# Kernel tuning notes

Measured on AMD Instinct MI355X. Metric: run time of the kernel, lower is better.

## Reference

```python
import jax, jax.numpy as jnp
import numpy as np

B, N, Mdim, CS, INP, OUT = 256, 2048, 64, 512, 256, 256
ADDR_R = Mdim + 6          # k(M), beta(1), g(1), s(3), gamma(1)
ADDR_W = 3 * Mdim + 6      # + erase(M) + add(M)


def setup_inputs() -> dict:
    key = jax.random.key(0)
    ks = jax.random.split(key, 16)
    s = 0.05
    x = jax.random.normal(ks[0], (B, INP), dtype=jnp.float32)
    memory = jax.random.uniform(ks[1], (B, N, Mdim), dtype=jnp.float32) * 0.1 + 1e-6
    h = jax.random.normal(ks[2], (B, CS), dtype=jnp.float32) * 0.1
    c = jax.random.normal(ks[3], (B, CS), dtype=jnp.float32) * 0.1
    rw = jax.random.uniform(ks[4], (B, N), dtype=jnp.float32)
    read_w = rw / rw.sum(axis=1, keepdims=True)
    ww = jax.random.uniform(ks[5], (B, N), dtype=jnp.float32)
    write_w = ww / ww.sum(axis=1, keepdims=True)
    prev_read = jax.random.normal(ks[6], (B, Mdim), dtype=jnp.float32) * 0.1
    W_ih = jax.random.normal(ks[7], (4 * CS, INP + Mdim), dtype=jnp.float32) * s
    W_hh = jax.random.normal(ks[8], (4 * CS, CS), dtype=jnp.float32) * s
    b_ih = jnp.zeros((4 * CS,), jnp.float32)
    b_hh = jnp.zeros((4 * CS,), jnp.float32)
    W_r = jax.random.normal(ks[9], (ADDR_R, CS), dtype=jnp.float32) * s
    b_r = jnp.zeros((ADDR_R,), jnp.float32)
    W_w = jax.random.normal(ks[10], (ADDR_W, CS), dtype=jnp.float32) * s
    b_w = jnp.zeros((ADDR_W,), jnp.float32)
    W_o = jax.random.normal(ks[11], (OUT, CS + Mdim), dtype=jnp.float32) * s
    b_o = jnp.zeros((OUT,), jnp.float32)
    return dict(x=x, memory=memory, h=h, c=c, read_w=read_w, write_w=write_w,
                prev_read=prev_read, W_ih=W_ih, W_hh=W_hh, b_ih=b_ih, b_hh=b_hh,
                W_r=W_r, b_r=b_r, W_w=W_w, b_w=b_w, W_o=W_o, b_o=b_o)


def _addressing(out_vec, prev_w, memory, M):
    # Eq. 5-9: content softmax, interpolation, circular shift, sharpening.
    k = out_vec[:, :M]                                   # [B, M]
    beta = jax.nn.softplus(out_vec[:, M:M + 1])          # [B, 1]
    g = jax.nn.sigmoid(out_vec[:, M + 1:M + 2])          # [B, 1]
    s = jax.nn.softmax(out_vec[:, M + 2:M + 5], axis=1)  # [B, 3]
    gamma = 1.0 + jax.nn.softplus(out_vec[:, M + 5:M + 6])
    norm_k = jnp.linalg.norm(k, axis=1, keepdims=True) + 1e-8        # [B, 1]
    norm_mem = jnp.linalg.norm(memory, axis=2) + 1e-8                # [B, N]
    sim = jnp.einsum('bnm,bm->bn', memory, k) / (norm_k * norm_mem)  # cosine
    w_c = jax.nn.softmax(beta * sim, axis=1)
    w_g = g * w_c + (1.0 - g) * prev_w
    # circular convolution with 3-tap shift kernel (replaces the roll loop)
    w_s = (s[:, 0:1] * jnp.roll(w_g, 1, axis=1)
           + s[:, 1:2] * w_g
           + s[:, 2:3] * jnp.roll(w_g, -1, axis=1))
    w_pow = w_s ** gamma
    return w_pow / (w_pow.sum(axis=1, keepdims=True) + 1e-8)


def reference(x, memory, h, c, read_w, write_w, prev_read,
              W_ih, W_hh, b_ih, b_hh, W_r, b_r, W_w, b_w, W_o, b_o):
    M = memory.shape[2]
    inp = jnp.concatenate([x, prev_read], axis=1)
    gates = inp @ W_ih.T + b_ih + h @ W_hh.T + b_hh
    i_g, f_g, g_g, o_g = jnp.split(gates, 4, axis=1)  # torch LSTMCell gate order
    i_g = jax.nn.sigmoid(i_g); f_g = jax.nn.sigmoid(f_g)
    g_g = jnp.tanh(g_g); o_g = jax.nn.sigmoid(o_g)
    c_new = f_g * c + i_g * g_g
    h_new = o_g * jnp.tanh(c_new)
    # read head (uses pre-write memory)
    read_out = h_new @ W_r.T + b_r
    w_read = _addressing(read_out, read_w, memory, M)
    read_vec = jnp.einsum('bn,bnm->bm', w_read, memory)
    # write head: address, then erase/add outer-product update
    write_out = h_new @ W_w.T + b_w
    w_write = _addressing(write_out, write_w, memory, M)
    erase = jax.nn.sigmoid(write_out[:, M + 6:2 * M + 6])
    add = write_out[:, 2 * M + 6:3 * M + 6]
    memory_new = memory * (1.0 - w_write[:, :, None] * erase[:, None, :]) \
                 + w_write[:, :, None] * add[:, None, :]
    out = jnp.concatenate([h_new, read_vec], axis=1) @ W_o.T + b_o
    return (out, memory_new, h_new, c_new, w_read, w_write, read_vec)
```

## Files before the change

kernel.cpp:

```cpp
#include <hip/hip_runtime.h>
#include <math.h>

#define Bsz   256
#define Nn    2048
#define Md    64
#define CSd   512
#define INPd  256
#define OUTd  256
#define KTOT  832
#define PSTRIDE 272
#define GSZ   524288
#define ZSPL  4
#define KZ    208

__device__ __forceinline__ float sigmoidf_(float x){ return 1.f/(1.f+expf(-x)); }
__device__ __forceinline__ float softplusf_(float x){ return fmaxf(x,0.f) + log1pf(expf(-fabsf(x))); }

__device__ __forceinline__ float4 loadA4(const float* __restrict__ x, const float* __restrict__ pr,
                                         const float* __restrict__ h, int row, int k){
  if (k < INPd)            return *(const float4*)&x[row*INPd + k];
  else if (k < INPd+Md)    return *(const float4*)&pr[row*Md + (k-INPd)];
  else                     return *(const float4*)&h[row*CSd + (k-INPd-Md)];
}
__device__ __forceinline__ float4 loadW4(const float* __restrict__ Wih, const float* __restrict__ Whh,
                                         int j, int k){
  if (k < INPd+Md)         return *(const float4*)&Wih[j*(INPd+Md) + k];
  else                     return *(const float4*)&Whh[j*CSd + (k-INPd-Md)];
}

__global__ __launch_bounds__(256) void k_gates(
    const float* __restrict__ x, const float* __restrict__ prev_read, const float* __restrict__ h,
    const float* __restrict__ W_ih, const float* __restrict__ W_hh,
    float* __restrict__ partials)
{
  __shared__ __align__(16) float As[16][68];
  __shared__ __align__(16) float Bs[16][68];
  const int t = threadIdx.x;
  const int col0 = blockIdx.x * 64;
  const int row0 = blockIdx.y * 64;
  const int z    = blockIdx.z;
  const int lr = t >> 2;
  const int kq = (t & 3) * 4;
  const int tr = t >> 4, tc = t & 15;
  const int arow = row0 + lr;
  const int bcol = col0 + lr;

  float acc[4][4] = {};
  int kb = z * KZ;
  float4 a  = loadA4(x, prev_read, h, arow, kb + kq);
  float4 bq = loadW4(W_ih, W_hh, bcol, kb + kq);

  for (int kc = 0; kc < 13; ++kc) {
    As[kq+0][lr] = a.x;  As[kq+1][lr] = a.y;  As[kq+2][lr] = a.z;  As[kq+3][lr] = a.w;
    Bs[kq+0][lr] = bq.x; Bs[kq+1][lr] = bq.y; Bs[kq+2][lr] = bq.z; Bs[kq+3][lr] = bq.w;
    __syncthreads();
    if (kc < 12) {
      int kn = kb + (kc+1)*16 + kq;
      a  = loadA4(x, prev_read, h, arow, kn);
      bq = loadW4(W_ih, W_hh, bcol, kn);
    }
    #pragma unroll
    for (int kk = 0; kk < 16; ++kk) {
      float av[4], bv[4];
      *(float4*)&av[0] = *(const float4*)&As[kk][tr*4];
      *(float4*)&bv[0] = *(const float4*)&Bs[kk][tc*4];
      #pragma unroll
      for (int i=0;i<4;++i)
        #pragma unroll
        for (int q=0;q<4;++q)
          acc[i][q] += av[i]*bv[q];
    }
    __syncthreads();
  }
  float* part = partials + (size_t)z * GSZ;
  #pragma unroll
  for (int i=0;i<4;++i) {
    int r = row0 + tr*4 + i;
    float4 v0 = {acc[i][0],acc[i][1],acc[i][2],acc[i][3]};
    *(float4*)&part[r*2048 + col0 + tc*4] = v0;
  }
}

__global__ __launch_bounds__(512) void k_lstm_heads(
    const float* __restrict__ partials, const float* __restrict__ c,
    const float* __restrict__ b_ih, const float* __restrict__ b_hh,
    const float* __restrict__ W_r, const float* __restrict__ b_r,
    const float* __restrict__ W_w, const float* __restrict__ b_w,
    float* __restrict__ h_new, float* __restrict__ c_new, float* __restrict__ params)
{
  __shared__ float hs[CSd];
  __shared__ float ob[268];
  int b = blockIdx.x, t = threadIdx.x;
  float g[4];
  #pragma unroll
  for (int q = 0; q < 4; ++q) {
    int col = q*512 + t;
    float s = b_ih[col] + b_hh[col];
    #pragma unroll
    for (int sp = 0; sp < ZSPL; ++sp) s += partials[(size_t)sp*GSZ + b*2048 + col];
    g[q] = s;
  }
  float ig = sigmoidf_(g[0]);
  float fg = sigmoidf_(g[1]);
  float gg = tanhf(g[2]);
  float og = sigmoidf_(g[3]);
  float cn = fg * c[b*CSd + t] + ig * gg;
  float hn = og * tanhf(cn);
  c_new[b*CSd + t] = cn;
  h_new[b*CSd + t] = hn;
  hs[t] = hn;
  __syncthreads();
  int wave = t >> 6, lane = t & 63;
  for (int r = wave; r < 268; r += 8) {
    const float* wrow; float bias;
    if (r < 70) { wrow = W_r + r*CSd;      bias = b_r[r]; }
    else        { wrow = W_w + (r-70)*CSd; bias = b_w[r-70]; }
    float s = 0.f;
    #pragma unroll
    for (int i = 0; i < 8; ++i) s += wrow[i*64 + lane] * hs[i*64 + lane];
    #pragma unroll
    for (int off = 32; off; off >>= 1) s += __shfl_xor(s, off);
    if (lane == 0) ob[r] = s + bias;
  }
  __syncthreads();
  float* P = params + b*PSTRIDE;
  if (t < 256) {
    if (t < 64)       P[t] = ob[t];
    else if (t < 128) P[t] = ob[70 + (t-64)];
    else if (t < 192) P[t] = sigmoidf_(ob[140 + (t-128)]);
    else              P[t] = ob[204 + (t-192)];
  }
  float* S = P + 256;
  if (wave == 0) {
    float v = ob[lane]; float sq = v*v;
    #pragma unroll
    for (int off = 32; off; off >>= 1) sq += __shfl_xor(sq, off);
    if (lane == 0) S[6] = 1.f/(sqrtf(sq)+1e-8f);
  } else if (wave == 1) {
    float v = ob[70 + lane]; float sq = v*v;
    #pragma unroll
    for (int off = 32; off; off >>= 1) sq += __shfl_xor(sq, off);
    if (lane == 0) S[13] = 1.f/(sqrtf(sq)+1e-8f);
  }
  if (t == 128) {
    S[0] = softplusf_(ob[64]);
    S[1] = sigmoidf_(ob[65]);
    float m3 = fmaxf(ob[66], fmaxf(ob[67], ob[68]));
    float e0=expf(ob[66]-m3), e1=expf(ob[67]-m3), e2=expf(ob[68]-m3);
    float es = e0+e1+e2;
    S[2]=e0/es; S[3]=e1/es; S[4]=e2/es;
    S[5] = 1.f + softplusf_(ob[69]);
  }
  if (t == 129) {
    S[7] = softplusf_(ob[134]);
    S[8] = sigmoidf_(ob[135]);
    float m3 = fmaxf(ob[136], fmaxf(ob[137], ob[138]));
    float e0=expf(ob[136]-m3), e1=expf(ob[137]-m3), e2=expf(ob[138]-m3);
    float es = e0+e1+e2;
    S[9]=e0/es; S[10]=e1/es; S[11]=e2/es;
    S[12] = 1.f + softplusf_(ob[139]);
  }
}

__global__ __launch_bounds__(256) void k_sim(
    const float* __restrict__ mem, const float* __restrict__ params,
    float* __restrict__ a_r, float* __restrict__ a_w)
{
  int b = blockIdx.y;
  int n0 = blockIdx.x * 64;
  int rr = threadIdx.x >> 4;
  int chunk = threadIdx.x & 15;
  const float* P = params + b*PSTRIDE;
  float4 kr = ((const float4*)P)[chunk];
  float4 kw = ((const float4*)(P+64))[chunk];
  const float* S = P + 256;
  float cr = S[0] * S[6];
  float cw = S[7] * S[13];
  #pragma unroll
  for (int p = 0; p < 4; ++p) {
    int n = n0 + p*16 + rr;
    float4 v = ((const float4*)mem)[(b*Nn + n)*16 + chunk];
    float ss = v.x*v.x + v.y*v.y + v.z*v.z + v.w*v.w;
    float pr = v.x*kr.x + v.y*kr.y + v.z*kr.z + v.w*kr.w;
    float pw = v.x*kw.x + v.y*kw.y + v.z*kw.z + v.w*kw.w;
    #pragma unroll
    for (int off=8; off; off>>=1) {
      ss += __shfl_xor(ss, off);
      pr += __shfl_xor(pr, off);
      pw += __shfl_xor(pw, off);
    }
    if (chunk == 0) {
      float inv_nm = 1.f/(sqrtf(ss)+1e-8f);
      a_r[b*Nn+n] = cr * pr * inv_nm;
      a_w[b*Nn+n] = cw * pw * inv_nm;
    }
  }
}

__device__ __forceinline__ float block_reduce512(float val, float* red, int t, bool ismax){
  #pragma unroll
  for (int off=32; off; off>>=1)
    val = ismax ? fmaxf(val, __shfl_xor(val,off)) : val + __shfl_xor(val,off);
  __syncthreads();
  if ((t&63)==0) red[t>>6] = val;
  __syncthreads();
  float r = red[0];
  if (ismax) { for (int i=1;i<8;++i) r = fmaxf(r, red[i]); }
  else       { for (int i=1;i<8;++i) r += red[i]; }
  return r;
}

__global__ __launch_bounds__(512) void k_weights(
    const float* __restrict__ a_r, const float* __restrict__ a_w,
    const float* __restrict__ read_w, const float* __restrict__ write_w,
    const float* __restrict__ params,
    float* __restrict__ w_read, float* __restrict__ w_write)
{
  __shared__ float wg[Nn];
  __shared__ float red[8];
  int b = blockIdx.x;
  int which = blockIdx.y;
  const float* a    = which ? a_w     : a_r;
  const float* prev = which ? write_w : read_w;
  float* outw       = which ? w_write : w_read;
  const float* S = params + b*PSTRIDE + 256 + (which ? 7 : 0);
  float g = S[1], s0 = S[2], s1 = S[3], s2 = S[4], gamma = S[5];
  int t = threadIdx.x;
  float v[4];
  #pragma unroll
  for (int i=0;i<4;++i) v[i] = a[b*Nn + t*4+i];
  float lmax = fmaxf(fmaxf(v[0],v[1]), fmaxf(v[2],v[3]));
  float mx = block_reduce512(lmax, red, t, true);
  float e[4]; float ps = 0.f;
  #pragma unroll
  for (int i=0;i<4;++i){ e[i] = expf(v[i]-mx); ps += e[i]; }
  float denom = block_reduce512(ps, red, t, false);
  float inv = 1.f/denom;
  #pragma unroll
  for (int i=0;i<4;++i){
    float wc = e[i]*inv;
    wg[t*4+i] = g*wc + (1.f-g)*prev[b*Nn + t*4+i];
  }
  __syncthreads();
  float wp[4]; float psum = 0.f;
  #pragma unroll
  for (int i=0;i<4;++i){
    int n = t*4+i;
    float wsv = s0*wg[(n+Nn-1)&(Nn-1)] + s1*wg[n] + s2*wg[(n+1)&(Nn-1)];
    wp[i] = powf(wsv, gamma);
    psum += wp[i];
  }
  float tot = block_reduce512(psum, red, t, false);
  float invt = 1.f/(tot + 1e-8f);
  #pragma unroll
  for (int i=0;i<4;++i) outw[b*Nn + t*4+i] = wp[i]*invt;
}

__global__ __launch_bounds__(256) void k_memupd(
    const float* __restrict__ mem, const float* __restrict__ params,
    const float* __restrict__ w_read, const float* __restrict__ w_write,
    float* __restrict__ mem_new, float* __restrict__ prv)
{
  __shared__ __align__(16) float er[64];
  __shared__ __align__(16) float ad[64];
  __shared__ float4 part[64];
  int b = blockIdx.y;
  int n0 = blockIdx.x * 64;
  int t = threadIdx.x;
  const float* P = params + b*PSTRIDE;
  if (t < 64)       er[t]    = P[128+t];
  else if (t < 128) ad[t-64] = P[192+(t-64)];
  __syncthreads();
  int chunk = t & 15;
  int rr = t >> 4;
  float4 e4 = ((const float4*)er)[chunk];
  float4 a4 = ((const float4*)ad)[chunk];
  float4 acc = {0.f,0.f,0.f,0.f};
  #pragma unroll
  for (int p = 0; p < 4; ++p) {
    int n = n0 + p*16 + rr;
    float4 v = ((const float4*)mem)[(b*Nn+n)*16 + chunk];
    float ww = w_write[b*Nn+n];
    float wr = w_read[b*Nn+n];
    float4 o;
    o.x = v.x*(1.f-ww*e4.x) + ww*a4.x;
    o.y = v.y*(1.f-ww*e4.y) + ww*a4.y;
    o.z = v.z*(1.f-ww*e4.z) + ww*a4.z;
    o.w = v.w*(1.f-ww*e4.w) + ww*a4.w;
    ((float4*)mem_new)[(b*Nn+n)*16 + chunk] = o;
    acc.x += wr*v.x; acc.y += wr*v.y; acc.z += wr*v.z; acc.w += wr*v.w;
  }
  #pragma unroll
  for (int off = 16; off <= 32; off <<= 1) {
    acc.x += __shfl_xor(acc.x, off);
    acc.y += __shfl_xor(acc.y, off);
    acc.z += __shfl_xor(acc.z, off);
    acc.w += __shfl_xor(acc.w, off);
  }
  int wave = t >> 6;
  if ((t & 63) < 16) part[wave*16 + chunk] = acc;
  __syncthreads();
  if (t < 16) {
    float4 s = part[t];
    for (int w=1; w<4; ++w){ float4 q = part[w*16+t]; s.x+=q.x; s.y+=q.y; s.z+=q.z; s.w+=q.w; }
    *(float4*)&prv[(b*32 + blockIdx.x)*64 + t*4] = s;
  }
}

__global__ __launch_bounds__(256) void k_out(
    const float* __restrict__ h_new, const float* __restrict__ prv,
    const float* __restrict__ W_o, const float* __restrict__ b_o,
    float* __restrict__ out, float* __restrict__ read_vec)
{
  __shared__ float vbuf[576];
  int b = blockIdx.y, t = threadIdx.x;
  vbuf[t]     = h_new[b*CSd + t];
  vbuf[t+256] = h_new[b*CSd + t + 256];
  if (t < 64) {
    float s = 0.f;
    #pragma unroll 8
    for (int i = 0; i < 32; ++i) s += prv[(b*32 + i)*64 + t];
    vbuf[512+t] = s;
    if (blockIdx.x == 0) read_vec[b*64 + t] = s;
  }
  __syncthreads();
  int wave = t >> 6, lane = t & 63;
  float vb[9];
  #pragma unroll
  for (int i = 0; i < 9; ++i) vb[i] = vbuf[i*64 + lane];
  int cbase = blockIdx.x*64 + wave*16;
  for (int jj = 0; jj < 16; ++jj) {
    int cc = cbase + jj;
    const float* w = W_o + cc*576;
    float s = 0.f;
    #pragma unroll
    for (int i = 0; i < 9; ++i) s += w[i*64 + lane] * vb[i];
    #pragma unroll
    for (int off = 32; off; off >>= 1) s += __shfl_xor(s, off);
    if (lane == 0) out[b*OUTd + cc] = s + b_o[cc];
  }
}

extern "C" void kernel_launch(void* const* d_in, const int* in_sizes, int n_in,
                              void* d_out, int out_size, void* d_ws, size_t ws_size,
                              hipStream_t stream)
{
  const float* x         = (const float*)d_in[0];
  const float* memory    = (const float*)d_in[1];
  const float* h         = (const float*)d_in[2];
  const float* c         = (const float*)d_in[3];
  const float* read_w    = (const float*)d_in[4];
  const float* write_w   = (const float*)d_in[5];
  const float* prev_read = (const float*)d_in[6];
  const float* W_ih      = (const float*)d_in[7];
  const float* W_hh      = (const float*)d_in[8];
  const float* b_ih      = (const float*)d_in[9];
  const float* b_hh      = (const float*)d_in[10];
  const float* W_r       = (const float*)d_in[11];
  const float* b_r       = (const float*)d_in[12];
  const float* W_w       = (const float*)d_in[13];
  const float* b_w       = (const float*)d_in[14];
  const float* W_o       = (const float*)d_in[15];
  const float* b_o       = (const float*)d_in[16];

  float* out      = (float*)d_out;
  float* mem_new  = out + 256*256;
  float* h_new    = mem_new + (size_t)256*2048*64;
  float* c_new    = h_new + 256*512;
  float* w_read   = c_new + 256*512;
  float* w_write  = w_read + 256*2048;
  float* read_vec = w_write + 256*2048;

  float* ws       = (float*)d_ws;
  float* params   = ws;
  float* partials = params + 256*PSTRIDE;
  float* a_r      = partials;
  float* a_w      = partials + GSZ;
  float* prv      = partials + 2*GSZ;

  k_gates     <<<dim3(32,4,ZSPL), 256, 0, stream>>>(x, prev_read, h, W_ih, W_hh, partials);
  k_lstm_heads<<<256,            512, 0, stream>>>(partials, c, b_ih, b_hh, W_r, b_r, W_w, b_w,
                                                   h_new, c_new, params);
  k_sim       <<<dim3(32,256),   256, 0, stream>>>(memory, params, a_r, a_w);
  k_weights   <<<dim3(256,2),    512, 0, stream>>>(a_r, a_w, read_w, write_w, params, w_read, w_write);
  k_memupd    <<<dim3(32,256),   256, 0, stream>>>(memory, params, w_read, w_write, mem_new, prv);
  k_out       <<<dim3(4,256),    256, 0, stream>>>(h_new, prv, W_o, b_o, out, read_vec);
}
```

Baseline: 365.9 us.

## Fuse LSTM, heads, addressing into one kernel and memory update with output

Merges the LSTM/head projection, content similarity and addressing softmax/shift/sharpen into a single per-batch kernel that keeps the similarity scores in shared memory. It also merges the memory erase/add update with the read-vector reduction and the output projection, and halves the gate GEMM split-K factor. This removes global round-trips for the similarity scores, the partial read vectors and the parameters, and cuts launches from six to three. The cost is only 256 blocks of 1024 threads for the memory-bound passes, which lowers parallelism and may reduce bandwidth utilisation.

```diff
diff --git a/kernel.cpp b/kernel.cpp
--- a/kernel.cpp
+++ b/kernel.cpp
@@ -8,10 +8,10 @@
 #define INPd  256
 #define OUTd  256
 #define KTOT  832
-#define PSTRIDE 272
+#define PSTRIDE 128
 #define GSZ   524288
-#define ZSPL  4
-#define KZ    208
+#define ZSPL  2
+#define KZ    416
 
 __device__ __forceinline__ float sigmoidf_(float x){ return 1.f/(1.f+expf(-x)); }
 __device__ __forceinline__ float softplusf_(float x){ return fmaxf(x,0.f) + log1pf(expf(-fabsf(x))); }
@@ -50,11 +50,11 @@
   float4 a  = loadA4(x, prev_read, h, arow, kb + kq);
   float4 bq = loadW4(W_ih, W_hh, bcol, kb + kq);
 
-  for (int kc = 0; kc < 13; ++kc) {
+  for (int kc = 0; kc < 26; ++kc) {
     As[kq+0][lr] = a.x;  As[kq+1][lr] = a.y;  As[kq+2][lr] = a.z;  As[kq+3][lr] = a.w;
     Bs[kq+0][lr] = bq.x; Bs[kq+1][lr] = bq.y; Bs[kq+2][lr] = bq.z; Bs[kq+3][lr] = bq.w;
     __syncthreads();
-    if (kc < 12) {
+    if (kc < 25) {
       int kn = kb + (kc+1)*16 + kq;
       a  = loadA4(x, prev_read, h, arow, kn);
       bq = loadW4(W_ih, W_hh, bcol, kn);
@@ -81,37 +81,63 @@
   }
 }
 
-__global__ __launch_bounds__(512) void k_lstm_heads(
+__device__ __forceinline__ float hreduce(float val, float* red, int t, bool ismax){
+  #pragma unroll
+  for (int off=32; off; off>>=1)
+    val = ismax ? fmaxf(val, __shfl_xor(val,off)) : val + __shfl_xor(val,off);
+  __syncthreads();
+  if ((t&63)==0) red[t>>6] = val;
+  __syncthreads();
+  int base = (t>>9)*8;
+  float r = red[base];
+  if (ismax) { for (int i=1;i<8;++i) r = fmaxf(r, red[base+i]); }
+  else       { for (int i=1;i<8;++i) r += red[base+i]; }
+  return r;
+}
+
+__global__ __launch_bounds__(1024) void k_fused(
     const float* __restrict__ partials, const float* __restrict__ c,
     const float* __restrict__ b_ih, const float* __restrict__ b_hh,
     const float* __restrict__ W_r, const float* __restrict__ b_r,
     const float* __restrict__ W_w, const float* __restrict__ b_w,
-    float* __restrict__ h_new, float* __restrict__ c_new, float* __restrict__ params)
+    const float* __restrict__ mem,
+    const float* __restrict__ read_w, const float* __restrict__ write_w,
+    float* __restrict__ h_new, float* __restrict__ c_new,
+    float* __restrict__ w_read, float* __restrict__ w_write,
+    float* __restrict__ params)
 {
-  __shared__ float hs[CSd];
+  __shared__ __align__(16) float hs[CSd];
   __shared__ float ob[268];
+  __shared__ __align__(16) float sim[2][Nn];
+  __shared__ float red[16];
+  __shared__ float sc[16];
+  __shared__ __align__(16) float kvec[128];
   int b = blockIdx.x, t = threadIdx.x;
-  float g[4];
-  #pragma unroll
-  for (int q = 0; q < 4; ++q) {
-    int col = q*512 + t;
-    float s = b_ih[col] + b_hh[col];
-    #pragma unroll
-    for (int sp = 0; sp < ZSPL; ++sp) s += partials[(size_t)sp*GSZ + b*2048 + col];
-    g[q] = s;
-  }
-  float ig = sigmoidf_(g[0]);
-  float fg = sigmoidf_(g[1]);
-  float gg = tanhf(g[2]);
-  float og = sigmoidf_(g[3]);
-  float cn = fg * c[b*CSd + t] + ig * gg;
-  float hn = og * tanhf(cn);
-  c_new[b*CSd + t] = cn;
-  h_new[b*CSd + t] = hn;
-  hs[t] = hn;
-  __syncthreads();
+
+  if (t < CSd) {
+    float g[4];
+    #pragma unroll
+    for (int q = 0; q < 4; ++q) {
+      int col = q*512 + t;
+      float s = b_ih[col] + b_hh[col];
+      #pragma unroll
+      for (int sp = 0; sp < ZSPL; ++sp) s += partials[(size_t)sp*GSZ + b*2048 + col];
+      g[q] = s;
+    }
+    float ig = sigmoidf_(g[0]);
+    float fg = sigmoidf_(g[1]);
+    float gg = tanhf(g[2]);
+    float og = sigmoidf_(g[3]);
+    float cn = fg * c[b*CSd + t] + ig * gg;
+    float hn = og * tanhf(cn);
+    c_new[b*CSd + t] = cn;
+    h_new[b*CSd + t] = hn;
+    hs[t] = hn;
+  }
+  __syncthreads();
+
   int wave = t >> 6, lane = t & 63;
-  for (int r = wave; r < 268; r += 8) {
+  for (int r = wave; r < 268; r += 16) {
     const float* wrow; float bias;
     if (r < 70) { wrow = W_r + r*CSd;      bias = b_r[r]; }
     else        { wrow = W_w + (r-70)*CSd; bias = b_w[r-70]; }
@@ -123,163 +149,142 @@
     if (lane == 0) ob[r] = s + bias;
   }
   __syncthreads();
-  float* P = params + b*PSTRIDE;
-  if (t < 256) {
-    if (t < 64)       P[t] = ob[t];
-    else if (t < 128) P[t] = ob[70 + (t-64)];
-    else if (t < 192) P[t] = sigmoidf_(ob[140 + (t-128)]);
-    else              P[t] = ob[204 + (t-192)];
-  }
-  float* S = P + 256;
+
   if (wave == 0) {
     float v = ob[lane]; float sq = v*v;
     #pragma unroll
     for (int off = 32; off; off >>= 1) sq += __shfl_xor(sq, off);
-    if (lane == 0) S[6] = 1.f/(sqrtf(sq)+1e-8f);
+    if (lane == 0) sc[6] = 1.f/(sqrtf(sq)+1e-8f);
   } else if (wave == 1) {
     float v = ob[70 + lane]; float sq = v*v;
     #pragma unroll
     for (int off = 32; off; off >>= 1) sq += __shfl_xor(sq, off);
-    if (lane == 0) S[13] = 1.f/(sqrtf(sq)+1e-8f);
+    if (lane == 0) sc[13] = 1.f/(sqrtf(sq)+1e-8f);
   }
   if (t == 128) {
-    S[0] = softplusf_(ob[64]);
-    S[1] = sigmoidf_(ob[65]);
+    sc[0] = softplusf_(ob[64]);
+    sc[1] = sigmoidf_(ob[65]);
     float m3 = fmaxf(ob[66], fmaxf(ob[67], ob[68]));
     float e0=expf(ob[66]-m3), e1=expf(ob[67]-m3), e2=expf(ob[68]-m3);
     float es = e0+e1+e2;
-    S[2]=e0/es; S[3]=e1/es; S[4]=e2/es;
-    S[5] = 1.f + softplusf_(ob[69]);
+    sc[2]=e0/es; sc[3]=e1/es; sc[4]=e2/es;
+    sc[5] = 1.f + softplusf_(ob[69]);
   }
   if (t == 129) {
-    S[7] = softplusf_(ob[134]);
-    S[8] = sigmoidf_(ob[135]);
+    sc[7] = softplusf_(ob[134]);
+    sc[8] = sigmoidf_(ob[135]);
     float m3 = fmaxf(ob[136], fmaxf(ob[137], ob[138]));
     float e0=expf(ob[136]-m3), e1=expf(ob[137]-m3), e2=expf(ob[138]-m3);
     float es = e0+e1+e2;
-    S[9]=e0/es; S[10]=e1/es; S[11]=e2/es;
-    S[12] = 1.f + softplusf_(ob[139]);
-  }
-}
-
-__global__ __launch_bounds__(256) void k_sim(
-    const float* __restrict__ mem, const float* __restrict__ params,
-    float* __restrict__ a_r, float* __restrict__ a_w)
-{
-  int b = blockIdx.y;
-  int n0 = blockIdx.x * 64;
-  int rr = threadIdx.x >> 4;
-  int chunk = threadIdx.x & 15;
-  const float* P = params + b*PSTRIDE;
-  float4 kr = ((const float4*)P)[chunk];
-  float4 kw = ((const float4*)(P+64))[chunk];
-  const float* S = P + 256;
-  float cr = S[0] * S[6];
-  float cw = S[7] * S[13];
-  #pragma unroll
-  for (int p = 0; p < 4; ++p) {
-    int n = n0 + p*16 + rr;
-    float4 v = ((const float4*)mem)[(b*Nn + n)*16 + chunk];
-    float ss = v.x*v.x + v.y*v.y + v.z*v.z + v.w*v.w;
-    float pr = v.x*kr.x + v.y*kr.y + v.z*kr.z + v.w*kr.w;
-    float pw = v.x*kw.x + v.y*kw.y + v.z*kw.z + v.w*kw.w;
-    #pragma unroll
-    for (int off=8; off; off>>=1) {
-      ss += __shfl_xor(ss, off);
-      pr += __shfl_xor(pr, off);
-      pw += __shfl_xor(pw, off);
-    }
-    if (chunk == 0) {
-      float inv_nm = 1.f/(sqrtf(ss)+1e-8f);
-      a_r[b*Nn+n] = cr * pr * inv_nm;
-      a_w[b*Nn+n] = cw * pw * inv_nm;
-    }
-  }
-}
-
-__device__ __forceinline__ float block_reduce512(float val, float* red, int t, bool ismax){
-  #pragma unroll
-  for (int off=32; off; off>>=1)
-    val = ismax ? fmaxf(val, __shfl_xor(val,off)) : val + __shfl_xor(val,off);
-  __syncthreads();
-  if ((t&63)==0) red[t>>6] = val;
-  __syncthreads();
-  float r = red[0];
-  if (ismax) { for (int i=1;i<8;++i) r = fmaxf(r, red[i]); }
-  else       { for (int i=1;i<8;++i) r += red[i]; }
-  return r;
-}
-
-__global__ __launch_bounds__(512) void k_weights(
-    const float* __restrict__ a_r, const float* __restrict__ a_w,
-    const float* __restrict__ read_w, const float* __restrict__ write_w,
-    const float* __restrict__ params,
-    float* __restrict__ w_read, float* __restrict__ w_write)
-{
-  __shared__ float wg[Nn];
-  __shared__ float red[8];
-  int b = blockIdx.x;
-  int which = blockIdx.y;
-  const float* a    = which ? a_w     : a_r;
-  const float* prev = which ? write_w : read_w;
-  float* outw       = which ? w_write : w_read;
-  const float* S = params + b*PSTRIDE + 256 + (which ? 7 : 0);
-  float g = S[1], s0 = S[2], s1 = S[3], s2 = S[4], gamma = S[5];
-  int t = threadIdx.x;
-  float v[4];
-  #pragma unroll
-  for (int i=0;i<4;++i) v[i] = a[b*Nn + t*4+i];
-  float lmax = fmaxf(fmaxf(v[0],v[1]), fmaxf(v[2],v[3]));
-  float mx = block_reduce512(lmax, red, t, true);
-  float e[4]; float ps = 0.f;
-  #pragma unroll
-  for (int i=0;i<4;++i){ e[i] = expf(v[i]-mx); ps += e[i]; }
-  float denom = block_reduce512(ps, red, t, false);
-  float inv = 1.f/denom;
-  #pragma unroll
-  for (int i=0;i<4;++i){
-    float wc = e[i]*inv;
-    wg[t*4+i] = g*wc + (1.f-g)*prev[b*Nn + t*4+i];
-  }
-  __syncthreads();
-  float wp[4]; float psum = 0.f;
-  #pragma unroll
-  for (int i=0;i<4;++i){
-    int n = t*4+i;
-    float wsv = s0*wg[(n+Nn-1)&(Nn-1)] + s1*wg[n] + s2*wg[(n+1)&(Nn-1)];
-    wp[i] = powf(wsv, gamma);
-    psum += wp[i];
-  }
-  float tot = block_reduce512(psum, red, t, false);
-  float invt = 1.f/(tot + 1e-8f);
-  #pragma unroll
-  for (int i=0;i<4;++i) outw[b*Nn + t*4+i] = wp[i]*invt;
-}
-
-__global__ __launch_bounds__(256) void k_memupd(
+    sc[9]=e0/es; sc[10]=e1/es; sc[11]=e2/es;
+    sc[12] = 1.f + softplusf_(ob[139]);
+  }
+  if (t >= 256 && t < 384) {
+    int i = t - 256;
+    kvec[i] = (i < 64) ? ob[i] : ob[70 + (i-64)];
+  }
+  if (t >= 384 && t < 512) {
+    int i = t - 384;
+    params[b*PSTRIDE + i] = (i < 64) ? sigmoidf_(ob[140+i]) : ob[204 + (i-64)];
+  }
+  __syncthreads();
+
+  {
+    int rr = t >> 4, chunk = t & 15;
+    float4 kr = ((const float4*)kvec)[chunk];
+    float4 kw = ((const float4*)(kvec+64))[chunk];
+    float cr = sc[0]*sc[6];
+    float cw = sc[7]*sc[13];
+    #pragma unroll 4
+    for (int p = 0; p < 32; ++p) {
+      int n = p*64 + rr;
+      float4 v = ((const float4*)mem)[((size_t)b*Nn + n)*16 + chunk];
+      float ss = v.x*v.x + v.y*v.y + v.z*v.z + v.w*v.w;
+      float pr = v.x*kr.x + v.y*kr.y + v.z*kr.z + v.w*kr.w;
+      float pw = v.x*kw.x + v.y*kw.y + v.z*kw.z + v.w*kw.w;
+      #pragma unroll
+      for (int off=8; off; off>>=1) {
+        ss += __shfl_xor(ss, off);
+        pr += __shfl_xor(pr, off);
+        pw += __shfl_xor(pw, off);
+      }
+      if (chunk == 0) {
+        float inv_nm = 1.f/(sqrtf(ss)+1e-8f);
+        sim[0][n] = cr * pr * inv_nm;
+        sim[1][n] = cw * pw * inv_nm;
+      }
+    }
+  }
+  __syncthreads();
+
+  {
+    int which = t >> 9;
+    int tt = t & 511;
+    const float* prev = which ? (write_w + b*Nn) : (read_w + b*Nn);
+    float* outw       = which ? (w_write + b*Nn) : (w_read + b*Nn);
+    const float* S = sc + which*7;
+    float g = S[1], s0 = S[2], s1 = S[3], s2 = S[4], gamma = S[5];
+    float4 v4 = *(const float4*)&sim[which][tt*4];
+    float v[4] = {v4.x, v4.y, v4.z, v4.w};
+    float lmax = fmaxf(fmaxf(v[0],v[1]), fmaxf(v[2],v[3]));
+    float mx = hreduce(lmax, red, t, true);
+    float e[4]; float ps = 0.f;
+    #pragma unroll
+    for (int i=0;i<4;++i){ e[i] = expf(v[i]-mx); ps += e[i]; }
+    float denom = hreduce(ps, red, t, false);
+    float inv = 1.f/denom;
+    float4 p4 = ((const float4*)prev)[tt];
+    float pv[4] = {p4.x, p4.y, p4.z, p4.w};
+    float* wg = sim[which];
+    #pragma unroll
+    for (int i=0;i<4;++i){
+      float wc = e[i]*inv;
+      wg[tt*4+i] = g*wc + (1.f-g)*pv[i];
+    }
+    __syncthreads();
+    float wp[4]; float psum = 0.f;
+    #pragma unroll
+    for (int i=0;i<4;++i){
+      int n = tt*4+i;
+      float wsv = s0*wg[(n+Nn-1)&(Nn-1)] + s1*wg[n] + s2*wg[(n+1)&(Nn-1)];
+      wp[i] = powf(wsv, gamma);
+      psum += wp[i];
+    }
+    float tot = hreduce(psum, red, t, false);
+    float invt = 1.f/(tot + 1e-8f);
+    float4 o4 = {wp[0]*invt, wp[1]*invt, wp[2]*invt, wp[3]*invt};
+    ((float4*)outw)[tt] = o4;
+  }
+}
+
+__global__ __launch_bounds__(1024) void k_mo(
     const float* __restrict__ mem, const float* __restrict__ params,
     const float* __restrict__ w_read, const float* __restrict__ w_write,
-    float* __restrict__ mem_new, float* __restrict__ prv)
+    const float* __restrict__ h_new,
+    const float* __restrict__ W_o, const float* __restrict__ b_o,
+    float* __restrict__ mem_new, float* __restrict__ read_vec, float* __restrict__ out)
 {
   __shared__ __align__(16) float er[64];
   __shared__ __align__(16) float ad[64];
-  __shared__ float4 part[64];
-  int b = blockIdx.y;
-  int n0 = blockIdx.x * 64;
-  int t = threadIdx.x;
+  __shared__ __align__(16) float4 part[16][16];
+  __shared__ __align__(16) float vbuf[576];
+  int b = blockIdx.x, t = threadIdx.x;
   const float* P = params + b*PSTRIDE;
-  if (t < 64)       er[t]    = P[128+t];
-  else if (t < 128) ad[t-64] = P[192+(t-64)];
-  __syncthreads();
+  if (t < 64)       er[t]    = P[t];
+  else if (t < 128) ad[t-64] = P[64+(t-64)];
+  if (t < CSd) vbuf[t] = h_new[b*CSd + t];
+  __syncthreads();
+
   int chunk = t & 15;
   int rr = t >> 4;
+  int wave = t >> 6, lane = t & 63;
   float4 e4 = ((const float4*)er)[chunk];
   float4 a4 = ((const float4*)ad)[chunk];
   float4 acc = {0.f,0.f,0.f,0.f};
-  #pragma unroll
-  for (int p = 0; p < 4; ++p) {
-    int n = n0 + p*16 + rr;
-    float4 v = ((const float4*)mem)[(b*Nn+n)*16 + chunk];
+  #pragma unroll 4
+  for (int p = 0; p < 32; ++p) {
+    int n = p*64 + rr;
+    float4 v = ((const float4*)mem)[((size_t)b*Nn+n)*16 + chunk];
     float ww = w_write[b*Nn+n];
     float wr = w_read[b*Nn+n];
     float4 o;
@@ -287,7 +292,7 @@
     o.y = v.y*(1.f-ww*e4.y) + ww*a4.y;
     o.z = v.z*(1.f-ww*e4.z) + ww*a4.z;
     o.w = v.w*(1.f-ww*e4.w) + ww*a4.w;
-    ((float4*)mem_new)[(b*Nn+n)*16 + chunk] = o;
+    ((float4*)mem_new)[((size_t)b*Nn+n)*16 + chunk] = o;
     acc.x += wr*v.x; acc.y += wr*v.y; acc.z += wr*v.z; acc.w += wr*v.w;
   }
   #pragma unroll
@@ -297,40 +302,23 @@
     acc.z += __shfl_xor(acc.z, off);
     acc.w += __shfl_xor(acc.w, off);
   }
-  int wave = t >> 6;
-  if ((t & 63) < 16) part[wave*16 + chunk] = acc;
-  __syncthreads();
+  if (lane < 16) part[wave][chunk] = acc;
+  __syncthreads();
+
   if (t < 16) {
-    float4 s = part[t];
-    for (int w=1; w<4; ++w){ float4 q = part[w*16+t]; s.x+=q.x; s.y+=q.y; s.z+=q.z; s.w+=q.w; }
-    *(float4*)&prv[(b*32 + blockIdx.x)*64 + t*4] = s;
-  }
-}
-
-__global__ __launch_bounds__(256) void k_out(
-    const float* __restrict__ h_new, const float* __restrict__ prv,
-    const float* __restrict__ W_o, const float* __restrict__ b_o,
-    float* __restrict__ out, float* __restrict__ read_vec)
-{
-  __shared__ float vbuf[576];
-  int b = blockIdx.y, t = threadIdx.x;
-  vbuf[t]     = h_new[b*CSd + t];
-  vbuf[t+256] = h_new[b*CSd + t + 256];
-  if (t < 64) {
-    float s = 0.f;
-    #pragma unroll 8
-    for (int i = 0; i < 32; ++i) s += prv[(b*32 + i)*64 + t];
-    vbuf[512+t] = s;
-    if (blockIdx.x == 0) read_vec[b*64 + t] = s;
-  }
-  __syncthreads();
-  int wave = t >> 6, lane = t & 63;
+    float4 s = part[0][t];
+    #pragma unroll
+    for (int w=1; w<16; ++w){ float4 q = part[w][t]; s.x+=q.x; s.y+=q.y; s.z+=q.z; s.w+=q.w; }
+    *(float4*)&vbuf[512 + t*4] = s;
+    *(float4*)&read_vec[b*64 + t*4] = s;
+  }
+  __syncthreads();
+
   float vb[9];
   #pragma unroll
   for (int i = 0; i < 9; ++i) vb[i] = vbuf[i*64 + lane];
-  int cbase = blockIdx.x*64 + wave*16;
   for (int jj = 0; jj < 16; ++jj) {
-    int cc = cbase + jj;
+    int cc = wave*16 + jj;
     const float* w = W_o + cc*576;
     float s = 0.f;
     #pragma unroll
@@ -374,15 +362,11 @@
   float* ws       = (float*)d_ws;
   float* params   = ws;
   float* partials = params + 256*PSTRIDE;
-  float* a_r      = partials;
-  float* a_w      = partials + GSZ;
-  float* prv      = partials + 2*GSZ;
-
-  k_gates     <<<dim3(32,4,ZSPL), 256, 0, stream>>>(x, prev_read, h, W_ih, W_hh, partials);
-  k_lstm_heads<<<256,            512, 0, stream>>>(partials, c, b_ih, b_hh, W_r, b_r, W_w, b_w,
-                                                   h_new, c_new, params);
-  k_sim       <<<dim3(32,256),   256, 0, stream>>>(memory, params, a_r, a_w);
-  k_weights   <<<dim3(256,2),    512, 0, stream>>>(a_r, a_w, read_w, write_w, params, w_read, w_write);
-  k_memupd    <<<dim3(32,256),   256, 0, stream>>>(memory, params, w_read, w_write, mem_new, prv);
-  k_out       <<<dim3(4,256),    256, 0, stream>>>(h_new, prv, W_o, b_o, out, read_vec);
-}
+
+  k_gates<<<dim3(32,4,ZSPL), 256, 0, stream>>>(x, prev_read, h, W_ih, W_hh, partials);
+  k_fused<<<256, 1024, 0, stream>>>(partials, c, b_ih, b_hh, W_r, b_r, W_w, b_w,
+                                    memory, read_w, write_w,
+                                    h_new, c_new, w_read, w_write, params);
+  k_mo   <<<256, 1024, 0, stream>>>(memory, params, w_read, w_write, h_new,
+                                    W_o, b_o, mem_new, read_vec, out);
+}
```

New measurement: 358.8 us. About the same (-1.9%).
